# Kernel tuning notes

Hardware: AMD Instinct MI355X
Metric: run time of the kernel (lower is better)

## Reference

```python
import jax, jax.numpy as jnp
import numpy as np

N = 100000
E = 1600000
G = 64  # number of graphs in batch
IN_DIM = 256
HID = 64
HEADS = 4
NUM_DOMAINS = 2
NEG_SLOPE = 0.2


def setup_inputs() -> dict:
    key = jax.random.key(0)
    ks = jax.random.split(key, 16)
    x = jax.random.normal(ks[0], (N, IN_DIM), dtype=jnp.float32)
    edge_index = jax.random.randint(ks[1], (2, E), 0, N, dtype=jnp.int64)
    batch = jnp.sort(jax.random.randint(ks[2], (N,), 0, G, dtype=jnp.int64))
    s = 1.0 / np.sqrt(IN_DIM)
    W1 = jax.random.uniform(ks[3], (IN_DIM, HEADS * HID), jnp.float32, -s, s)
    att_src1 = jax.random.normal(ks[4], (HEADS, HID), jnp.float32) * 0.1
    att_dst1 = jax.random.normal(ks[5], (HEADS, HID), jnp.float32) * 0.1
    b1 = jnp.zeros((HEADS * HID,), jnp.float32)
    s2 = 1.0 / np.sqrt(HEADS * HID)
    W2 = jax.random.uniform(ks[6], (HEADS * HID, HID), jnp.float32, -s2, s2)
    att_src2 = jax.random.normal(ks[7], (1, HID), jnp.float32) * 0.1
    att_dst2 = jax.random.normal(ks[8], (1, HID), jnp.float32) * 0.1
    b2 = jnp.zeros((HID,), jnp.float32)
    s3 = 1.0 / np.sqrt(HID)
    W3 = jax.random.uniform(ks[9], (HID, HID // 2), jnp.float32, -s3, s3)
    b3 = jnp.zeros((HID // 2,), jnp.float32)
    s4 = 1.0 / np.sqrt(HID // 2)
    W4 = jax.random.uniform(ks[10], (HID // 2, NUM_DOMAINS), jnp.float32, -s4, s4)
    b4 = jnp.zeros((NUM_DOMAINS,), jnp.float32)
    return dict(x=x, edge_index=edge_index, batch=batch,
                W1=W1, att_src1=att_src1, att_dst1=att_dst1, b1=b1,
                W2=W2, att_src2=att_src2, att_dst2=att_dst2, b2=b2,
                W3=W3, b3=b3, W4=W4, b4=b4)


def gat_conv(x, src, dst, W, att_src, att_dst, bias, concat):
    # PyG GATConv (dropout inactive in eval mode)
    H, C = att_src.shape
    h = (x @ W).reshape(N, H, C)                      # [N,H,C]
    a_src = jnp.sum(h * att_src, axis=-1)             # [N,H]
    a_dst = jnp.sum(h * att_dst, axis=-1)             # [N,H]
    alpha = jax.nn.leaky_relu(a_src[src] + a_dst[dst], NEG_SLOPE)  # [E',H]
    amax = jax.ops.segment_max(alpha, dst, num_segments=N)
    alpha = jnp.exp(alpha - amax[dst])
    denom = jax.ops.segment_sum(alpha, dst, num_segments=N)
    alpha = alpha / (denom[dst] + 1e-16)              # segment softmax over incoming edges
    msg = h[src] * alpha[..., None]                   # [E',H,C]
    out = jax.ops.segment_sum(msg, dst, num_segments=N)  # [N,H,C]
    if concat:
        return out.reshape(N, H * C) + bias
    return out.mean(axis=1) + bias


def reference(x, edge_index, batch,
              W1, att_src1, att_dst1, b1,
              W2, att_src2, att_dst2, b2,
              W3, b3, W4, b4):
    # GRL is identity in forward
    loops = jnp.arange(N, dtype=edge_index.dtype)
    src = jnp.concatenate([edge_index[0], loops])  # add_self_loops (PyG default)
    dst = jnp.concatenate([edge_index[1], loops])
    h = jax.nn.elu(gat_conv(x, src, dst, W1, att_src1, att_dst1, b1, concat=True))
    h = gat_conv(h, src, dst, W2, att_src2, att_dst2, b2, concat=False)  # [N,HID]
    # global mean pool over graphs
    sums = jax.ops.segment_sum(h, batch, num_segments=G)
    cnt = jax.ops.segment_sum(jnp.ones((N,), h.dtype), batch, num_segments=G)
    graph_emb = sums / jnp.maximum(cnt, 1.0)[:, None]  # [G,HID]
    z = jax.nn.relu(graph_emb @ W3 + b3)
    logits = z @ W4 + b4                                # [G,NUM_DOMAINS]
    return logits
```

## Files before the change

### kernel.cpp

```cpp
#include <hip/hip_runtime.h>
#include <math.h>

#define N_NODES 100000
#define E_EDGES 1600000
#define E_TOT   (E_EDGES + N_NODES)
#define G_GRAPHS 64
#define IN_DIM 256
#define HID 64
#define HEADS 4
#define D1 256
#define NEG_SLOPE 0.2f
#define SCAN_B 1024
#define CHUNK2 8

typedef float nfloat4 __attribute__((ext_vector_type(4)));
typedef unsigned short nus4 __attribute__((ext_vector_type(4)));
typedef short bf16x8 __attribute__((ext_vector_type(8)));
typedef float f32x4 __attribute__((ext_vector_type(4)));

__device__ __forceinline__ float bf2f(unsigned short u) {
    unsigned int t = ((unsigned int)u) << 16;
    return __builtin_bit_cast(float, t);
}
__device__ __forceinline__ unsigned short f2bf(float f) {
    unsigned int u = __builtin_bit_cast(unsigned int, f);
    u += 0x7FFF + ((u >> 16) & 1);
    return (unsigned short)(u >> 16);
}
__device__ __forceinline__ unsigned int pk2(float lo, float hi) {
    unsigned int ul = __builtin_bit_cast(unsigned int, lo) + 0x8000u;
    unsigned int uh = __builtin_bit_cast(unsigned int, hi) + 0x8000u;
    return __builtin_amdgcn_perm(uh, ul, 0x07060302u);
}

__device__ __forceinline__ void packW(const float* __restrict__ W,
                                      unsigned short* __restrict__ Wpk, int Nc, int t)
{
    int kg = t / Nc, n = t - kg * Nc;
    const float* p = W + (size_t)(kg * 8) * Nc + n;
    uint4 v;
    v.x = pk2(p[0],      p[Nc]);
    v.y = pk2(p[2 * Nc], p[3 * Nc]);
    v.z = pk2(p[4 * Nc], p[5 * Nc]);
    v.w = pk2(p[6 * Nc], p[7 * Nc]);
    *(uint4*)(Wpk + (size_t)t * 8) = v;
}
__global__ __launch_bounds__(256) void convW2x(const float* __restrict__ W1,
                                               unsigned short* __restrict__ Wpk1,
                                               const float* __restrict__ W2,
                                               unsigned short* __restrict__ Wpk2)
{
    int t = blockIdx.x * 256 + threadIdx.x;
    if (t < 32 * D1) packW(W1, Wpk1, D1, t);
    else if (t < 32 * D1 + 32 * HID) packW(W2, Wpk2, HID, t - 32 * D1);
}

template<int BN, bool ABF16, bool CFP8>
__global__ __launch_bounds__(256) void gemm_mfma(const void* __restrict__ Ain,
                                                 const unsigned short* __restrict__ Wpk,
                                                 void* __restrict__ C,
                                                 int Nc,
                                                 const float* __restrict__ att_src,
                                                 const float* __restrict__ att_dst,
                                                 float* __restrict__ a_srcO,
                                                 float* __restrict__ a_dstO,
                                                 int astride)
{
    constexpr int NCG = BN / 16;
    __shared__ unsigned short alds[2][4][128][8];
    const int tid = threadIdx.x;
    const int lane = tid & 63, wv = tid >> 6;
    const int qd = lane >> 4, c16 = lane & 15;
    const int bm = blockIdx.y * 128, bn = blockIdx.x * BN;

    f32x4 acc[2][NCG];
#pragma unroll
    for (int i = 0; i < 2; ++i)
#pragma unroll
        for (int j = 0; j < NCG; ++j) acc[i][j] = (f32x4){0.f, 0.f, 0.f, 0.f};

    const int ar = tid >> 1, akh = tid & 1;
    const int gm = bm + ar;
    const bool mv = gm < N_NODES;

    uint4 v0, v1;
    float4 f0, f1, f2, f3;
    if (ABF16) {
        const unsigned short* Ab = (const unsigned short*)Ain + (size_t)gm * 256 + akh * 16;
        v0 = mv ? *(const uint4*)Ab : make_uint4(0, 0, 0, 0);
        v1 = mv ? *(const uint4*)(Ab + 8) : make_uint4(0, 0, 0, 0);
    } else {
        const float* Af = (const float*)Ain + (size_t)gm * 256 + akh * 16;
        if (mv) { f0 = ((const float4*)Af)[0]; f1 = ((const float4*)Af)[1];
                  f2 = ((const float4*)Af)[2]; f3 = ((const float4*)Af)[3]; }
        else { f0 = f1 = f2 = f3 = make_float4(0.f, 0.f, 0.f, 0.f); }
    }

    for (int k0 = 0; k0 < 256; k0 += 32) {
        const int p = (k0 >> 5) & 1;
        if (ABF16) {
            *(uint4*)&alds[p][2 * akh][ar][0] = v0;
            *(uint4*)&alds[p][2 * akh + 1][ar][0] = v1;
        } else {
            uint4 p0 = make_uint4(pk2(f0.x, f0.y), pk2(f0.z, f0.w), pk2(f1.x, f1.y), pk2(f1.z, f1.w));
            uint4 p1 = make_uint4(pk2(f2.x, f2.y), pk2(f2.z, f2.w), pk2(f3.x, f3.y), pk2(f3.z, f3.w));
            *(uint4*)&alds[p][2 * akh][ar][0] = p0;
            *(uint4*)&alds[p][2 * akh + 1][ar][0] = p1;
        }
        __syncthreads();

        if (k0 + 32 < 256) {
            if (ABF16) {
                const unsigned short* Ab = (const unsigned short*)Ain + (size_t)gm * 256 + (k0 + 32) + akh * 16;
                v0 = mv ? *(const uint4*)Ab : make_uint4(0, 0, 0, 0);
                v1 = mv ? *(const uint4*)(Ab + 8) : make_uint4(0, 0, 0, 0);
            } else {
                const float* Af = (const float*)Ain + (size_t)gm * 256 + (k0 + 32) + akh * 16;
                if (mv) { f0 = ((const float4*)Af)[0]; f1 = ((const float4*)Af)[1];
                          f2 = ((const float4*)Af)[2]; f3 = ((const float4*)Af)[3]; }
            }
        }

        const unsigned short* Wq = Wpk + ((size_t)((k0 >> 3) + qd) * Nc + bn) * 8;
        bf16x8 af0 = *(const bf16x8*)&alds[p][qd][wv * 32 + c16][0];
        bf16x8 af1 = *(const bf16x8*)&alds[p][qd][wv * 32 + 16 + c16][0];
#pragma unroll
        for (int cg = 0; cg < NCG; ++cg) {
            bf16x8 bfr = *(const bf16x8*)(Wq + (size_t)(cg * 16 + c16) * 8);
            acc[0][cg] = __builtin_amdgcn_mfma_f32_16x16x32_bf16(af0, bfr, acc[0][cg], 0, 0, 0);
            acc[1][cg] = __builtin_amdgcn_mfma_f32_16x16x32_bf16(af1, bfr, acc[1][cg], 0, 0, 0);
        }
    }

    float sv[NCG], dv[NCG];
#pragma unroll
    for (int cg = 0; cg < NCG; ++cg) {
        sv[cg] = att_src[bn + cg * 16 + c16];
        dv[cg] = att_dst[bn + cg * 16 + c16];
    }
#pragma unroll
    for (int rg = 0; rg < 2; ++rg) {
#pragma unroll
        for (int reg = 0; reg < 4; ++reg) {
            const int m = bm + wv * 32 + rg * 16 + qd * 4 + reg;
#pragma unroll
            for (int hh = 0; hh < NCG / 4; ++hh) {
                float ps = 0.f, pd = 0.f;
#pragma unroll
                for (int cg = 4 * hh; cg < 4 * hh + 4; ++cg) {
                    ps += acc[rg][cg][reg] * sv[cg];
                    pd += acc[rg][cg][reg] * dv[cg];
                }
#pragma unroll
                for (int o = 1; o < 16; o <<= 1) { ps += __shfl_xor(ps, o); pd += __shfl_xor(pd, o); }
                if (c16 == 0 && m < N_NODES) {
                    a_srcO[m * astride + (bn >> 6) + hh] = ps;
                    a_dstO[m * astride + (bn >> 6) + hh] = pd;
                }
            }
            if (m < N_NODES) {
#pragma unroll
                for (int cg = 0; cg < NCG; ++cg) {
                    float val = acc[rg][cg][reg];
                    if (CFP8) {
                        unsigned int q = (unsigned int)__builtin_amdgcn_cvt_pk_fp8_f32(val, val, 0, false);
                        ((unsigned char*)C)[(size_t)m * Nc + bn + cg * 16 + c16] = (unsigned char)q;
                    } else {
                        ((unsigned short*)C)[(size_t)m * Nc + bn + cg * 16 + c16] = f2bf(val);
                    }
                }
            }
        }
    }
}

__global__ void edge_hist(const int* __restrict__ ei, int* __restrict__ deg,
                          int* __restrict__ rank)
{
    for (int e = blockIdx.x * blockDim.x + threadIdx.x; e < E_TOT; e += gridDim.x * blockDim.x) {
        int d = (e < E_EDGES) ? ei[E_EDGES + e] : (e - E_EDGES);
        rank[e] = atomicAdd(&deg[d], 1);
    }
}

__global__ __launch_bounds__(SCAN_B) void scan_block(const int* __restrict__ deg,
                                                     int* __restrict__ incl,
                                                     int* __restrict__ bsum, int n)
{
    __shared__ int s[SCAN_B];
    int i = blockIdx.x * SCAN_B + threadIdx.x;
    int v = (i < n) ? deg[i] : 0;
    s[threadIdx.x] = v;
    __syncthreads();
    for (int off = 1; off < SCAN_B; off <<= 1) {
        int t = (threadIdx.x >= off) ? s[threadIdx.x - off] : 0;
        __syncthreads();
        s[threadIdx.x] += t;
        __syncthreads();
    }
    if (i < n) incl[i] = s[threadIdx.x];
    if (threadIdx.x == SCAN_B - 1) bsum[blockIdx.x] = s[SCAN_B - 1];
}

__global__ void scan_bsum(const int* __restrict__ bsum, int* __restrict__ bex, int nb)
{
    __shared__ int s[128];
    int i = threadIdx.x;
    int v = (i < nb) ? bsum[i] : 0;
    s[i] = v;
    __syncthreads();
    for (int off = 1; off < 128; off <<= 1) {
        int t = (i >= off) ? s[i - off] : 0;
        __syncthreads();
        s[i] += t;
        __syncthreads();
    }
    if (i < nb) bex[i] = s[i] - v;
}

__global__ void finalize_off(const int* __restrict__ deg, const int* __restrict__ incl,
                             const int* __restrict__ bex, int* __restrict__ off, int n)
{
    int i = blockIdx.x * blockDim.x + threadIdx.x;
    if (i < n) off[i] = incl[i] - deg[i] + bex[i / SCAN_B];
}

__global__ void edge_scatter(const int* __restrict__ ei, const int* __restrict__ off,
                             const int* __restrict__ rank, int* __restrict__ csr_src)
{
    for (int e = blockIdx.x * blockDim.x + threadIdx.x; e < E_TOT; e += gridDim.x * blockDim.x) {
        int s = (e < E_EDGES) ? ei[e] : (e - E_EDGES);
        int d = (e < E_EDGES) ? ei[E_EDGES + e] : (e - E_EDGES);
        csr_src[off[d] + rank[e]] = s;
    }
}

__global__ __launch_bounds__(256) void agg1_kernel(const unsigned char* __restrict__ h1b,
                                                   const int* __restrict__ csr_src,
                                                   const int* __restrict__ off,
                                                   const int* __restrict__ deg,
                                                   const float* __restrict__ a_src,
                                                   const float* __restrict__ a_dst,
                                                   const float* __restrict__ b1,
                                                   unsigned short* __restrict__ hEb)
{
    __shared__ int s_sh[4][72];
    __shared__ __align__(16) float ex_sh[4][72][4];
    const int wv = threadIdx.x >> 6, lane = threadIdx.x & 63;
    const int n = blockIdx.x * 4 + wv;
    if (n >= N_NODES) return;
    const int h = lane >> 4;
    const int st = off[n], cnt = deg[n];
    const float4 ad4 = *(const float4*)(a_dst + (size_t)n * 4);

    float4 acc = make_float4(0.f, 0.f, 0.f, 0.f);
    float dsum = 0.f;
    const unsigned char* __restrict__ hb = h1b + lane * 4;

    for (int cb = 0; cb < cnt; cb += 64) {
        const int c0 = st + cb;
        const int m = (cnt - cb < 64) ? (cnt - cb) : 64;

        {
            int s_l = csr_src[c0 + ((lane < m) ? lane : 0)];
            float4 as4 = *(const float4*)(a_src + (size_t)s_l * 4);
            float e0 = as4.x + ad4.x, e1 = as4.y + ad4.y,
                  e2 = as4.z + ad4.z, e3 = as4.w + ad4.w;
            e0 = (e0 > 0.f) ? e0 : NEG_SLOPE * e0;
            e1 = (e1 > 0.f) ? e1 : NEG_SLOPE * e1;
            e2 = (e2 > 0.f) ? e2 : NEG_SLOPE * e2;
            e3 = (e3 > 0.f) ? e3 : NEG_SLOPE * e3;
            float4 exv;
            exv.x = __expf(e0); exv.y = __expf(e1);
            exv.z = __expf(e2); exv.w = __expf(e3);
            if (lane < m) {
                s_sh[wv][lane] = s_l;
                *(float4*)&ex_sh[wv][lane][0] = exv;
            }
            if (lane < 8) {
                s_sh[wv][m + lane] = csr_src[c0];
                *(float4*)&ex_sh[wv][m + lane][0] = make_float4(0.f, 0.f, 0.f, 0.f);
            }
        }

        const int m4 = (m + 3) & ~3;
        int   sR0 = s_sh[wv][0], sR1 = s_sh[wv][1], sR2 = s_sh[wv][2], sR3 = s_sh[wv][3];
        float eR0 = ex_sh[wv][0][h], eR1 = ex_sh[wv][1][h],
              eR2 = ex_sh[wv][2][h], eR3 = ex_sh[wv][3][h];
        unsigned int vR0 = *(const unsigned int*)(hb + (size_t)sR0 * D1);
        unsigned int vR1 = *(const unsigned int*)(hb + (size_t)sR1 * D1);
        unsigned int vR2 = *(const unsigned int*)(hb + (size_t)sR2 * D1);
        unsigned int vR3 = *(const unsigned int*)(hb + (size_t)sR3 * D1);
        for (int j = 0; j < m4; j += 4) {
            int   sN0 = s_sh[wv][j + 4], sN1 = s_sh[wv][j + 5],
                  sN2 = s_sh[wv][j + 6], sN3 = s_sh[wv][j + 7];
            float eN0 = ex_sh[wv][j + 4][h], eN1 = ex_sh[wv][j + 5][h],
                  eN2 = ex_sh[wv][j + 6][h], eN3 = ex_sh[wv][j + 7][h];
            unsigned int vN0 = *(const unsigned int*)(hb + (size_t)sN0 * D1);
            unsigned int vN1 = *(const unsigned int*)(hb + (size_t)sN1 * D1);
            unsigned int vN2 = *(const unsigned int*)(hb + (size_t)sN2 * D1);
            unsigned int vN3 = *(const unsigned int*)(hb + (size_t)sN3 * D1);

            dsum += eR0;
            acc.x += eR0 * __builtin_amdgcn_cvt_f32_fp8((int)vR0, 0);
            acc.y += eR0 * __builtin_amdgcn_cvt_f32_fp8((int)vR0, 1);
            acc.z += eR0 * __builtin_amdgcn_cvt_f32_fp8((int)vR0, 2);
            acc.w += eR0 * __builtin_amdgcn_cvt_f32_fp8((int)vR0, 3);
            dsum += eR1;
            acc.x += eR1 * __builtin_amdgcn_cvt_f32_fp8((int)vR1, 0);
            acc.y += eR1 * __builtin_amdgcn_cvt_f32_fp8((int)vR1, 1);
            acc.z += eR1 * __builtin_amdgcn_cvt_f32_fp8((int)vR1, 2);
            acc.w += eR1 * __builtin_amdgcn_cvt_f32_fp8((int)vR1, 3);
            dsum += eR2;
            acc.x += eR2 * __builtin_amdgcn_cvt_f32_fp8((int)vR2, 0);
            acc.y += eR2 * __builtin_amdgcn_cvt_f32_fp8((int)vR2, 1);
            acc.z += eR2 * __builtin_amdgcn_cvt_f32_fp8((int)vR2, 2);
            acc.w += eR2 * __builtin_amdgcn_cvt_f32_fp8((int)vR2, 3);
            dsum += eR3;
            acc.x += eR3 * __builtin_amdgcn_cvt_f32_fp8((int)vR3, 0);
            acc.y += eR3 * __builtin_amdgcn_cvt_f32_fp8((int)vR3, 1);
            acc.z += eR3 * __builtin_amdgcn_cvt_f32_fp8((int)vR3, 2);
            acc.w += eR3 * __builtin_amdgcn_cvt_f32_fp8((int)vR3, 3);

            sR0 = sN0; sR1 = sN1; sR2 = sN2; sR3 = sN3;
            eR0 = eN0; eR1 = eN1; eR2 = eN2; eR3 = eN3;
            vR0 = vN0; vR1 = vN1; vR2 = vN2; vR3 = vN3;
        }
    }

    const float inv = 1.f / (dsum + 1e-16f);
    float4 bb = *(const float4*)(b1 + lane * 4);
    float ox = acc.x * inv + bb.x;
    float oy = acc.y * inv + bb.y;
    float oz = acc.z * inv + bb.z;
    float ow = acc.w * inv + bb.w;
    ox = (ox > 0.f) ? ox : expm1f(ox);
    oy = (oy > 0.f) ? oy : expm1f(oy);
    oz = (oz > 0.f) ? oz : expm1f(oz);
    ow = (ow > 0.f) ? ow : expm1f(ow);
    nus4 ob = { f2bf(ox), f2bf(oy), f2bf(oz), f2bf(ow) };
    __builtin_nontemporal_store(ob, (nus4*)(hEb + (size_t)n * D1 + lane * 4));
}

__global__ __launch_bounds__(256) void agg2_pool_kernel(const unsigned short* __restrict__ h2b,
                                                        const int* __restrict__ csr_src,
                                                        const int* __restrict__ off,
                                                        const int* __restrict__ deg,
                                                        const float* __restrict__ a_src,
                                                        const float* __restrict__ a_dst,
                                                        const float* __restrict__ b2,
                                                        const int* __restrict__ batch,
                                                        float* __restrict__ pool,
                                                        float* __restrict__ cntg)
{
    __shared__ int   s_sh[4][2][80];
    __shared__ float ex_sh[4][2][80];
    const int wv = threadIdx.x >> 6, lane = threadIdx.x & 63;
    const int q = lane >> 4, ql = lane & 15;
    const int f0 = ql * 4;
    const int wgid = blockIdx.x * 4 + wv;
    const int n0 = wgid * CHUNK2;
    if (n0 >= N_NODES) return;
    const int n1 = (n0 + CHUNK2 < N_NODES) ? n0 + CHUNK2 : N_NODES;
    const float4 bb = *(const float4*)(b2 + f0);
    const unsigned short* __restrict__ hb = h2b + f0;

    float4 pacc = make_float4(0.f, 0.f, 0.f, 0.f);
    float ccur = 0.f;
    int gcur = batch[n0];
    int buf = 0;

    int stP = off[n0], cntP = deg[n0];
    float adP = a_dst[n0];
    {
        const int mP = (cntP < 64) ? cntP : 64;
        int s_l = csr_src[stP + ((lane < mP) ? lane : 0)];
        float a = a_src[s_l] + adP;
        a = (a > 0.f) ? a : NEG_SLOPE * a;
        float ex = __expf(a);
        if (lane < mP) { s_sh[wv][0][lane] = s_l; ex_sh[wv][0][lane] = ex; }
        int sb = __shfl(s_l, 0);
        if (lane < 16) { s_sh[wv][0][mP + lane] = sb; ex_sh[wv][0][mP + lane] = 0.f; }
    }

    for (int n = n0; n < n1; ++n) {
        const int st = stP, cnt = cntP;
        const float adn = adP;

        const bool hasN = (n + 1 < n1);
        int stN = 0, cntN = 0, sN = 0; float aN = 0.f, adN = 0.f;
        if (hasN) {
            stN = off[n + 1]; cntN = deg[n + 1]; adN = a_dst[n + 1];
            const int mN = (cntN < 64) ? cntN : 64;
            sN = csr_src[stN + ((lane < mN) ? lane : 0)];
            aN = a_src[sN];
        }

        float4 acc = make_float4(0.f, 0.f, 0.f, 0.f);
        float dsum = 0.f;

        for (int cb = 0; cb < cnt; cb += 64) {
            const int m = (cnt - cb < 64) ? (cnt - cb) : 64;
            if (cb > 0) {
                int s_l = csr_src[st + cb + ((lane < m) ? lane : 0)];
                float a = a_src[s_l] + adn;
                a = (a > 0.f) ? a : NEG_SLOPE * a;
                float ex = __expf(a);
                if (lane < m) { s_sh[wv][buf][lane] = s_l; ex_sh[wv][buf][lane] = ex; }
                int sb = __shfl(s_l, 0);
                if (lane < 16) { s_sh[wv][buf][m + lane] = sb; ex_sh[wv][buf][m + lane] = 0.f; }
            }

            const int m4 = (m + 3) & ~3;
            int   sA = s_sh[wv][buf][q],      sB = s_sh[wv][buf][q + 4],  sC = s_sh[wv][buf][q + 8];
            float eA = ex_sh[wv][buf][q],     eB = ex_sh[wv][buf][q + 4], eC = ex_sh[wv][buf][q + 8];
            ushort4 vA = *(const ushort4*)(hb + (size_t)sA * HID);
            ushort4 vB = *(const ushort4*)(hb + (size_t)sB * HID);
            ushort4 vC = *(const ushort4*)(hb + (size_t)sC * HID);
            for (int j = 0; j < m4; j += 4) {
                int   sD = s_sh[wv][buf][j + 12 + q];
                float eD = ex_sh[wv][buf][j + 12 + q];
                ushort4 vD = *(const ushort4*)(hb + (size_t)sD * HID);

                dsum += eA;
                acc.x += eA * bf2f(vA.x); acc.y += eA * bf2f(vA.y);
                acc.z += eA * bf2f(vA.z); acc.w += eA * bf2f(vA.w);

                sA = sB; eA = eB; vA = vB;
                sB = sC; eB = eC; vB = vC;
                sC = sD; eC = eD; vC = vD;
            }
        }

        if (hasN) {
            const int mN = (cntN < 64) ? cntN : 64;
            float a = aN + adN;
            a = (a > 0.f) ? a : NEG_SLOPE * a;
            float ex = __expf(a);
            if (lane < mN) { s_sh[wv][buf ^ 1][lane] = sN; ex_sh[wv][buf ^ 1][lane] = ex; }
            int sb = __shfl(sN, 0);
            if (lane < 16) { s_sh[wv][buf ^ 1][mN + lane] = sb; ex_sh[wv][buf ^ 1][mN + lane] = 0.f; }
        }

        dsum  += __shfl_xor(dsum, 16);  dsum  += __shfl_xor(dsum, 32);
        acc.x += __shfl_xor(acc.x, 16); acc.x += __shfl_xor(acc.x, 32);
        acc.y += __shfl_xor(acc.y, 16); acc.y += __shfl_xor(acc.y, 32);
        acc.z += __shfl_xor(acc.z, 16); acc.z += __shfl_xor(acc.z, 32);
        acc.w += __shfl_xor(acc.w, 16); acc.w += __shfl_xor(acc.w, 32);

        const float inv = 1.f / (dsum + 1e-16f);
        float4 v;
        v.x = acc.x * inv + bb.x;
        v.y = acc.y * inv + bb.y;
        v.z = acc.z * inv + bb.z;
        v.w = acc.w * inv + bb.w;

        int g = batch[n];
        if (g != gcur) {
            if (q == 0) {
#if defined(__AMDGCN__)
                unsafeAtomicAdd(&pool[gcur * HID + f0 + 0], pacc.x);
                unsafeAtomicAdd(&pool[gcur * HID + f0 + 1], pacc.y);
                unsafeAtomicAdd(&pool[gcur * HID + f0 + 2], pacc.z);
                unsafeAtomicAdd(&pool[gcur * HID + f0 + 3], pacc.w);
                if (ql == 0) unsafeAtomicAdd(&cntg[gcur], ccur);
#else
                atomicAdd(&pool[gcur * HID + f0 + 0], pacc.x);
                atomicAdd(&pool[gcur * HID + f0 + 1], pacc.y);
                atomicAdd(&pool[gcur * HID + f0 + 2], pacc.z);
                atomicAdd(&pool[gcur * HID + f0 + 3], pacc.w);
                if (ql == 0) atomicAdd(&cntg[gcur], ccur);
#endif
            }
            pacc = make_float4(0.f, 0.f, 0.f, 0.f); ccur = 0.f; gcur = g;
        }
        pacc.x += v.x; pacc.y += v.y; pacc.z += v.z; pacc.w += v.w;
        ccur += 1.f;

        stP = stN; cntP = cntN; adP = adN; buf ^= 1;
    }
    if (q == 0) {
#if defined(__AMDGCN__)
        unsafeAtomicAdd(&pool[gcur * HID + f0 + 0], pacc.x);
        unsafeAtomicAdd(&pool[gcur * HID + f0 + 1], pacc.y);
        unsafeAtomicAdd(&pool[gcur * HID + f0 + 2], pacc.z);
        unsafeAtomicAdd(&pool[gcur * HID + f0 + 3], pacc.w);
        if (ql == 0) unsafeAtomicAdd(&cntg[gcur], ccur);
#else
        atomicAdd(&pool[gcur * HID + f0 + 0], pacc.x);
        atomicAdd(&pool[gcur * HID + f0 + 1], pacc.y);
        atomicAdd(&pool[gcur * HID + f0 + 2], pacc.z);
        atomicAdd(&pool[gcur * HID + f0 + 3], pacc.w);
        if (ql == 0) atomicAdd(&cntg[gcur], ccur);
#endif
    }
}

__global__ __launch_bounds__(64) void head_kernel(const float* __restrict__ pool,
                                                  const float* __restrict__ cntg,
                                                  const float* __restrict__ W3,
                                                  const float* __restrict__ b3,
                                                  const float* __restrict__ W4,
                                                  const float* __restrict__ b4,
                                                  float* __restrict__ out)
{
    const int g = blockIdx.x;
    const int lane = threadIdx.x;
    const float invc = 1.f / fmaxf(cntg[g], 1.f);
    float z = 0.f;
    if (lane < 32) {
        z = b3[lane];
        for (int k = 0; k < HID; ++k)
            z += pool[g * HID + k] * invc * W3[k * 32 + lane];
        z = fmaxf(z, 0.f);
    }
    float p0 = (lane < 32) ? z * W4[lane * 2 + 0] : 0.f;
    float p1 = (lane < 32) ? z * W4[lane * 2 + 1] : 0.f;
#pragma unroll
    for (int o = 1; o < 32; o <<= 1) { p0 += __shfl_xor(p0, o); p1 += __shfl_xor(p1, o); }
    if (lane == 0) { out[g * 2 + 0] = b4[0] + p0; out[g * 2 + 1] = b4[1] + p1; }
}

extern "C" void kernel_launch(void* const* d_in, const int* in_sizes, int n_in,
                              void* d_out, int out_size, void* d_ws, size_t ws_size,
                              hipStream_t stream)
{
    const float* x     = (const float*)d_in[0];
    const int*   ei    = (const int*)d_in[1];
    const int*   batch = (const int*)d_in[2];
    const float* W1    = (const float*)d_in[3];
    const float* as1w  = (const float*)d_in[4];
    const float* ad1w  = (const float*)d_in[5];
    const float* b1    = (const float*)d_in[6];
    const float* W2    = (const float*)d_in[7];
    const float* as2w  = (const float*)d_in[8];
    const float* ad2w  = (const float*)d_in[9];
    const float* b2    = (const float*)d_in[10];
    const float* W3    = (const float*)d_in[11];
    const float* b3    = (const float*)d_in[12];
    const float* W4    = (const float*)d_in[13];
    const float* b4    = (const float*)d_in[14];
    float* out = (float*)d_out;

    char* ws = (char*)d_ws;
    size_t o = 0;
    auto alloc = [&](size_t bytes) -> void* {
        void* p = ws + o;
        o += (bytes + 255) & ~(size_t)255;
        return p;
    };
    unsigned char*  h1b = (unsigned char*)alloc((size_t)N_NODES * D1);
    unsigned short* hEb = (unsigned short*)alloc((size_t)N_NODES * D1 * 2);
    unsigned short* h2b = (unsigned short*)alloc((size_t)N_NODES * HID * 2);
    float* a_s1 = (float*)alloc((size_t)N_NODES * 4 * 4);
    float* a_d1 = (float*)alloc((size_t)N_NODES * 4 * 4);
    float* a_s2 = (float*)alloc((size_t)N_NODES * 4);
    float* a_d2 = (float*)alloc((size_t)N_NODES * 4);
    char*  zbase  = (char*)alloc((size_t)N_NODES * 4 + G_GRAPHS * HID * 4 + G_GRAPHS * 4 + 1024);
    int*   deg    = (int*)zbase;
    float* pool   = (float*)(zbase + (((size_t)N_NODES * 4 + 255) & ~(size_t)255));
    float* cntg   = (float*)((char*)pool + (((size_t)G_GRAPHS * HID * 4 + 255) & ~(size_t)255));
    size_t zspan  = (char*)(cntg + G_GRAPHS) - zbase;
    int*   incl   = (int*)alloc((size_t)N_NODES * 4);
    int*   offv   = (int*)alloc((size_t)N_NODES * 4);
    int*   rank   = (int*)alloc((size_t)E_TOT * 4);
    int*   bsum   = (int*)alloc(128 * 4);
    int*   bex    = (int*)alloc(128 * 4);
    int*   csr    = (int*)alloc((size_t)E_TOT * 4);
    unsigned short* Wpk1 = (unsigned short*)alloc((size_t)32 * D1 * 8 * 2);
    unsigned short* Wpk2 = (unsigned short*)alloc((size_t)32 * HID * 8 * 2);

    (void)hipMemsetAsync(zbase, 0, zspan, stream);

    const int nblk_nodes = (N_NODES + 3) / 4;
    const int nscan = (N_NODES + SCAN_B - 1) / SCAN_B;
    const int nrowblk = (N_NODES + 127) / 128;

    convW2x<<<(32 * D1 + 32 * HID + 255) / 256, 256, 0, stream>>>(W1, Wpk1, W2, Wpk2);

    gemm_mfma<128, false, true><<<dim3(2, nrowblk), 256, 0, stream>>>(
        x, Wpk1, h1b, D1, as1w, ad1w, a_s1, a_d1, 4);

    edge_hist<<<4096, 256, 0, stream>>>(ei, deg, rank);
    scan_block<<<nscan, SCAN_B, 0, stream>>>(deg, incl, bsum, N_NODES);
    scan_bsum<<<1, 128, 0, stream>>>(bsum, bex, nscan);
    finalize_off<<<(N_NODES + 255) / 256, 256, 0, stream>>>(deg, incl, bex, offv, N_NODES);
    edge_scatter<<<4096, 256, 0, stream>>>(ei, offv, rank, csr);

    agg1_kernel<<<nblk_nodes, 256, 0, stream>>>(h1b, csr, offv, deg, a_s1, a_d1, b1, hEb);

    gemm_mfma<64, true, false><<<dim3(1, nrowblk), 256, 0, stream>>>(
        hEb, Wpk2, h2b, HID, as2w, ad2w, a_s2, a_d2, 1);

    const int nwaves2 = (N_NODES + CHUNK2 - 1) / CHUNK2;
    agg2_pool_kernel<<<(nwaves2 + 3) / 4, 256, 0, stream>>>(h2b, csr, offv, deg, a_s2, a_d2, b2, batch, pool, cntg);

    head_kernel<<<G_GRAPHS, 64, 0, stream>>>(pool, cntg, W3, b3, W4, b4, out);
}
```

Before: 584.8 us.

## Software-pipeline layer-2 gather across nodes with two-deep index prefetch

Restructures the agg2_pool kernel so that the first 32 neighbor payload rows of the next node are gathered into registers while the current node is accumulated. CSR indices and attention logits are prefetched two nodes ahead. The shared padding grows to 32 slots so these fixed-size loads stay in bounds. The aim is to hide gather latency across node boundaries, at the cost of more registers and wasted loads for low-degree nodes.

```diff
diff --git a/kernel.cpp b/kernel.cpp
--- a/kernel.cpp
+++ b/kernel.cpp
@@ -353,8 +353,8 @@
                                                         float* __restrict__ pool,
                                                         float* __restrict__ cntg)
 {
-    __shared__ int   s_sh[4][2][80];
-    __shared__ float ex_sh[4][2][80];
+    __shared__ int   s_sh[4][2][96];
+    __shared__ float ex_sh[4][2][96];
     const int wv = threadIdx.x >> 6, lane = threadIdx.x & 63;
     const int q = lane >> 4, ql = lane & 15;
     const int f0 = ql * 4;
@@ -370,76 +370,137 @@
     int gcur = batch[n0];
     int buf = 0;
 
-    int stP = off[n0], cntP = deg[n0];
-    float adP = a_dst[n0];
+    int stC = off[n0], cntC = deg[n0];
+    float adC = a_dst[n0];
     {
-        const int mP = (cntP < 64) ? cntP : 64;
-        int s_l = csr_src[stP + ((lane < mP) ? lane : 0)];
-        float a = a_src[s_l] + adP;
+        const int m = (cntC < 64) ? cntC : 64;
+        int s_l = csr_src[stC + ((lane < m) ? lane : 0)];
+        float a = a_src[s_l] + adC;
         a = (a > 0.f) ? a : NEG_SLOPE * a;
         float ex = __expf(a);
-        if (lane < mP) { s_sh[wv][0][lane] = s_l; ex_sh[wv][0][lane] = ex; }
+        if (lane < m) { s_sh[wv][0][lane] = s_l; ex_sh[wv][0][lane] = ex; }
         int sb = __shfl(s_l, 0);
-        if (lane < 16) { s_sh[wv][0][mP + lane] = sb; ex_sh[wv][0][mP + lane] = 0.f; }
+        if (lane < 32) { s_sh[wv][0][m + lane] = sb; ex_sh[wv][0][m + lane] = 0.f; }
+    }
+    ushort4 pay0, pay1, pay2, pay3, pay4, pay5, pay6, pay7;
+    {
+        int t0 = s_sh[wv][0][q], t1 = s_sh[wv][0][q + 4], t2 = s_sh[wv][0][q + 8], t3 = s_sh[wv][0][q + 12];
+        int t4 = s_sh[wv][0][q + 16], t5 = s_sh[wv][0][q + 20], t6 = s_sh[wv][0][q + 24], t7 = s_sh[wv][0][q + 28];
+        pay0 = *(const ushort4*)(hb + (size_t)t0 * HID);
+        pay1 = *(const ushort4*)(hb + (size_t)t1 * HID);
+        pay2 = *(const ushort4*)(hb + (size_t)t2 * HID);
+        pay3 = *(const ushort4*)(hb + (size_t)t3 * HID);
+        pay4 = *(const ushort4*)(hb + (size_t)t4 * HID);
+        pay5 = *(const ushort4*)(hb + (size_t)t5 * HID);
+        pay6 = *(const ushort4*)(hb + (size_t)t6 * HID);
+        pay7 = *(const ushort4*)(hb + (size_t)t7 * HID);
+    }
+
+    int stN = 0, cntN = 0, sNl = 0; float adN = 0.f, aNl = 0.f;
+    if (n0 + 1 < n1) {
+        stN = off[n0 + 1]; cntN = deg[n0 + 1]; adN = a_dst[n0 + 1];
+        const int mN = (cntN < 64) ? cntN : 64;
+        sNl = csr_src[stN + ((lane < mN) ? lane : 0)];
+        aNl = a_src[sNl];
     }
 
     for (int n = n0; n < n1; ++n) {
-        const int st = stP, cnt = cntP;
-        const float adn = adP;
-
+        const int st = stC, cnt = cntC;
+        const float adn = adC;
         const bool hasN = (n + 1 < n1);
-        int stN = 0, cntN = 0, sN = 0; float aN = 0.f, adN = 0.f;
+        const bool hasN2 = (n + 2 < n1);
+
+        int stN2 = 0, cntN2 = 0, sN2l = 0; float adN2 = 0.f, aN2l = 0.f;
+        if (hasN2) {
+            stN2 = off[n + 2]; cntN2 = deg[n + 2]; adN2 = a_dst[n + 2];
+            const int mN2 = (cntN2 < 64) ? cntN2 : 64;
+            sN2l = csr_src[stN2 + ((lane < mN2) ? lane : 0)];
+            aN2l = a_src[sN2l];
+        }
+
         if (hasN) {
-            stN = off[n + 1]; cntN = deg[n + 1]; adN = a_dst[n + 1];
             const int mN = (cntN < 64) ? cntN : 64;
-            sN = csr_src[stN + ((lane < mN) ? lane : 0)];
-            aN = a_src[sN];
+            float a = aNl + adN;
+            a = (a > 0.f) ? a : NEG_SLOPE * a;
+            float ex = __expf(a);
+            if (lane < mN) { s_sh[wv][buf ^ 1][lane] = sNl; ex_sh[wv][buf ^ 1][lane] = ex; }
+            int sb = __shfl(sNl, 0);
+            if (lane < 32) { s_sh[wv][buf ^ 1][mN + lane] = sb; ex_sh[wv][buf ^ 1][mN + lane] = 0.f; }
+        }
+
+        ushort4 pn0, pn1, pn2, pn3, pn4, pn5, pn6, pn7;
+        if (hasN) {
+            const int* sp = &s_sh[wv][buf ^ 1][0];
+            int t0 = sp[q], t1 = sp[q + 4], t2 = sp[q + 8], t3 = sp[q + 12];
+            int t4 = sp[q + 16], t5 = sp[q + 20], t6 = sp[q + 24], t7 = sp[q + 28];
+            pn0 = *(const ushort4*)(hb + (size_t)t0 * HID);
+            pn1 = *(const ushort4*)(hb + (size_t)t1 * HID);
+            pn2 = *(const ushort4*)(hb + (size_t)t2 * HID);
+            pn3 = *(const ushort4*)(hb + (size_t)t3 * HID);
+            pn4 = *(const ushort4*)(hb + (size_t)t4 * HID);
+            pn5 = *(const ushort4*)(hb + (size_t)t5 * HID);
+            pn6 = *(const ushort4*)(hb + (size_t)t6 * HID);
+            pn7 = *(const ushort4*)(hb + (size_t)t7 * HID);
         }
 
         float4 acc = make_float4(0.f, 0.f, 0.f, 0.f);
         float dsum = 0.f;
-
-        for (int cb = 0; cb < cnt; cb += 64) {
+        {
+            const float* ep = &ex_sh[wv][buf][0];
+            float e0 = ep[q], e1 = ep[q + 4], e2 = ep[q + 8], e3 = ep[q + 12];
+            float e4 = ep[q + 16], e5 = ep[q + 20], e6 = ep[q + 24], e7 = ep[q + 28];
+            dsum += e0;
+            acc.x += e0 * bf2f(pay0.x); acc.y += e0 * bf2f(pay0.y);
+            acc.z += e0 * bf2f(pay0.z); acc.w += e0 * bf2f(pay0.w);
+            dsum += e1;
+            acc.x += e1 * bf2f(pay1.x); acc.y += e1 * bf2f(pay1.y);
+            acc.z += e1 * bf2f(pay1.z); acc.w += e1 * bf2f(pay1.w);
+            dsum += e2;
+            acc.x += e2 * bf2f(pay2.x); acc.y += e2 * bf2f(pay2.y);
+            acc.z += e2 * bf2f(pay2.z); acc.w += e2 * bf2f(pay2.w);
+            dsum += e3;
+            acc.x += e3 * bf2f(pay3.x); acc.y += e3 * bf2f(pay3.y);
+            acc.z += e3 * bf2f(pay3.z); acc.w += e3 * bf2f(pay3.w);
+            dsum += e4;
+            acc.x += e4 * bf2f(pay4.x); acc.y += e4 * bf2f(pay4.y);
+            acc.z += e4 * bf2f(pay4.z); acc.w += e4 * bf2f(pay4.w);
+            dsum += e5;
+            acc.x += e5 * bf2f(pay5.x); acc.y += e5 * bf2f(pay5.y);
+            acc.z += e5 * bf2f(pay5.z); acc.w += e5 * bf2f(pay5.w);
+            dsum += e6;
+            acc.x += e6 * bf2f(pay6.x); acc.y += e6 * bf2f(pay6.y);
+            acc.z += e6 * bf2f(pay6.z); acc.w += e6 * bf2f(pay6.w);
+            dsum += e7;
+            acc.x += e7 * bf2f(pay7.x); acc.y += e7 * bf2f(pay7.y);
+            acc.z += e7 * bf2f(pay7.z); acc.w += e7 * bf2f(pay7.w);
+        }
+        const int mC = (cnt < 64) ? cnt : 64;
+        for (int j = 32; j < mC; j += 4) {
+            int   s = s_sh[wv][buf][j + q];
+            float e = ex_sh[wv][buf][j + q];
+            ushort4 v = *(const ushort4*)(hb + (size_t)s * HID);
+            dsum += e;
+            acc.x += e * bf2f(v.x); acc.y += e * bf2f(v.y);
+            acc.z += e * bf2f(v.z); acc.w += e * bf2f(v.w);
+        }
+        for (int cb = 64; cb < cnt; cb += 64) {
             const int m = (cnt - cb < 64) ? (cnt - cb) : 64;
-            if (cb > 0) {
-                int s_l = csr_src[st + cb + ((lane < m) ? lane : 0)];
-                float a = a_src[s_l] + adn;
-                a = (a > 0.f) ? a : NEG_SLOPE * a;
-                float ex = __expf(a);
-                if (lane < m) { s_sh[wv][buf][lane] = s_l; ex_sh[wv][buf][lane] = ex; }
-                int sb = __shfl(s_l, 0);
-                if (lane < 16) { s_sh[wv][buf][m + lane] = sb; ex_sh[wv][buf][m + lane] = 0.f; }
-            }
-
-            const int m4 = (m + 3) & ~3;
-            int   sA = s_sh[wv][buf][q],      sB = s_sh[wv][buf][q + 4],  sC = s_sh[wv][buf][q + 8];
-            float eA = ex_sh[wv][buf][q],     eB = ex_sh[wv][buf][q + 4], eC = ex_sh[wv][buf][q + 8];
-            ushort4 vA = *(const ushort4*)(hb + (size_t)sA * HID);
-            ushort4 vB = *(const ushort4*)(hb + (size_t)sB * HID);
-            ushort4 vC = *(const ushort4*)(hb + (size_t)sC * HID);
-            for (int j = 0; j < m4; j += 4) {
-                int   sD = s_sh[wv][buf][j + 12 + q];
-                float eD = ex_sh[wv][buf][j + 12 + q];
-                ushort4 vD = *(const ushort4*)(hb + (size_t)sD * HID);
-
-                dsum += eA;
-                acc.x += eA * bf2f(vA.x); acc.y += eA * bf2f(vA.y);
-                acc.z += eA * bf2f(vA.z); acc.w += eA * bf2f(vA.w);
-
-                sA = sB; eA = eB; vA = vB;
-                sB = sC; eB = eC; vB = vC;
-                sC = sD; eC = eD; vC = vD;
-            }
-        }
-
-        if (hasN) {
-            const int mN = (cntN < 64) ? cntN : 64;
-            float a = aN + adN;
+            int s_l = csr_src[st + cb + ((lane < m) ? lane : 0)];
+            float a = a_src[s_l] + adn;
             a = (a > 0.f) ? a : NEG_SLOPE * a;
             float ex = __expf(a);
-            if (lane < mN) { s_sh[wv][buf ^ 1][lane] = sN; ex_sh[wv][buf ^ 1][lane] = ex; }
-            int sb = __shfl(sN, 0);
-            if (lane < 16) { s_sh[wv][buf ^ 1][mN + lane] = sb; ex_sh[wv][buf ^ 1][mN + lane] = 0.f; }
+            if (lane < m) { s_sh[wv][buf][lane] = s_l; ex_sh[wv][buf][lane] = ex; }
+            int sb = __shfl(s_l, 0);
+            if (lane < 32) { s_sh[wv][buf][m + lane] = sb; ex_sh[wv][buf][m + lane] = 0.f; }
+            const int m4 = (m + 3) & ~3;
+            for (int j = 0; j < m4; j += 4) {
+                int   s = s_sh[wv][buf][j + q];
+                float e = ex_sh[wv][buf][j + q];
+                ushort4 v = *(const ushort4*)(hb + (size_t)s * HID);
+                dsum += e;
+                acc.x += e * bf2f(v.x); acc.y += e * bf2f(v.y);
+                acc.z += e * bf2f(v.z); acc.w += e * bf2f(v.w);
+            }
         }
 
         dsum  += __shfl_xor(dsum, 16);  dsum  += __shfl_xor(dsum, 32);
@@ -477,7 +538,14 @@
         pacc.x += v.x; pacc.y += v.y; pacc.z += v.z; pacc.w += v.w;
         ccur += 1.f;
 
-        stP = stN; cntP = cntN; adP = adN; buf ^= 1;
+        stC = stN; cntC = cntN; adC = adN;
+        stN = stN2; cntN = cntN2; adN = adN2;
+        sNl = sN2l; aNl = aN2l;
+        if (hasN) {
+            pay0 = pn0; pay1 = pn1; pay2 = pn2; pay3 = pn3;
+            pay4 = pn4; pay5 = pn5; pay6 = pn6; pay7 = pn7;
+        }
+        buf ^= 1;
     }
     if (q == 0) {
 #if defined(__AMDGCN__)
```

After: 594.8 us. Within noise of the previous version (+1.7%).

## Split layer-2 aggregation and mean pooling into separate per-node and pool kernels

Applied to the files above, without the earlier changes.

The fused aggregation+pooling kernel, where each wave walked 8 nodes with software prefetch, is replaced by a one-wave-per-node aggregation kernel that writes fp32 node outputs to a new buffer. A separate pool kernel then sums those rows per graph with atomics. This aims for more parallelism and better latency hiding in the gather. In exchange it adds an extra kernel launch plus a 25.6MB write and reread, and drops the cross-node prefetch.

```diff
diff --git a/kernel.cpp b/kernel.cpp
--- a/kernel.cpp
+++ b/kernel.cpp
@@ -11,7 +11,6 @@
 #define D1 256
 #define NEG_SLOPE 0.2f
 #define SCAN_B 1024
-#define CHUNK2 8
 
 typedef float nfloat4 __attribute__((ext_vector_type(4)));
 typedef unsigned short nus4 __attribute__((ext_vector_type(4)));
@@ -342,158 +341,117 @@
     __builtin_nontemporal_store(ob, (nus4*)(hEb + (size_t)n * D1 + lane * 4));
 }
 
-__global__ __launch_bounds__(256) void agg2_pool_kernel(const unsigned short* __restrict__ h2b,
+__global__ __launch_bounds__(256) void agg2_node_kernel(const unsigned short* __restrict__ h2b,
                                                         const int* __restrict__ csr_src,
                                                         const int* __restrict__ off,
                                                         const int* __restrict__ deg,
                                                         const float* __restrict__ a_src,
                                                         const float* __restrict__ a_dst,
                                                         const float* __restrict__ b2,
-                                                        const int* __restrict__ batch,
-                                                        float* __restrict__ pool,
-                                                        float* __restrict__ cntg)
-{
-    __shared__ int   s_sh[4][2][80];
-    __shared__ float ex_sh[4][2][80];
+                                                        float* __restrict__ h3)
+{
+    __shared__ int   s_sh[4][96];
+    __shared__ float ex_sh[4][96];
     const int wv = threadIdx.x >> 6, lane = threadIdx.x & 63;
+    const int n = blockIdx.x * 4 + wv;
+    if (n >= N_NODES) return;
     const int q = lane >> 4, ql = lane & 15;
     const int f0 = ql * 4;
-    const int wgid = blockIdx.x * 4 + wv;
-    const int n0 = wgid * CHUNK2;
-    if (n0 >= N_NODES) return;
-    const int n1 = (n0 + CHUNK2 < N_NODES) ? n0 + CHUNK2 : N_NODES;
-    const float4 bb = *(const float4*)(b2 + f0);
+    const int st = off[n], cnt = deg[n];
+    const float adn = a_dst[n];
     const unsigned short* __restrict__ hb = h2b + f0;
 
-    float4 pacc = make_float4(0.f, 0.f, 0.f, 0.f);
-    float ccur = 0.f;
-    int gcur = batch[n0];
-    int buf = 0;
-
-    int stP = off[n0], cntP = deg[n0];
-    float adP = a_dst[n0];
-    {
-        const int mP = (cntP < 64) ? cntP : 64;
-        int s_l = csr_src[stP + ((lane < mP) ? lane : 0)];
-        float a = a_src[s_l] + adP;
-        a = (a > 0.f) ? a : NEG_SLOPE * a;
-        float ex = __expf(a);
-        if (lane < mP) { s_sh[wv][0][lane] = s_l; ex_sh[wv][0][lane] = ex; }
-        int sb = __shfl(s_l, 0);
-        if (lane < 16) { s_sh[wv][0][mP + lane] = sb; ex_sh[wv][0][mP + lane] = 0.f; }
-    }
-
-    for (int n = n0; n < n1; ++n) {
-        const int st = stP, cnt = cntP;
-        const float adn = adP;
-
-        const bool hasN = (n + 1 < n1);
-        int stN = 0, cntN = 0, sN = 0; float aN = 0.f, adN = 0.f;
-        if (hasN) {
-            stN = off[n + 1]; cntN = deg[n + 1]; adN = a_dst[n + 1];
-            const int mN = (cntN < 64) ? cntN : 64;
-            sN = csr_src[stN + ((lane < mN) ? lane : 0)];
-            aN = a_src[sN];
-        }
-
-        float4 acc = make_float4(0.f, 0.f, 0.f, 0.f);
-        float dsum = 0.f;
-
-        for (int cb = 0; cb < cnt; cb += 64) {
-            const int m = (cnt - cb < 64) ? (cnt - cb) : 64;
-            if (cb > 0) {
-                int s_l = csr_src[st + cb + ((lane < m) ? lane : 0)];
-                float a = a_src[s_l] + adn;
-                a = (a > 0.f) ? a : NEG_SLOPE * a;
-                float ex = __expf(a);
-                if (lane < m) { s_sh[wv][buf][lane] = s_l; ex_sh[wv][buf][lane] = ex; }
-                int sb = __shfl(s_l, 0);
-                if (lane < 16) { s_sh[wv][buf][m + lane] = sb; ex_sh[wv][buf][m + lane] = 0.f; }
-            }
-
-            const int m4 = (m + 3) & ~3;
-            int   sA = s_sh[wv][buf][q],      sB = s_sh[wv][buf][q + 4],  sC = s_sh[wv][buf][q + 8];
-            float eA = ex_sh[wv][buf][q],     eB = ex_sh[wv][buf][q + 4], eC = ex_sh[wv][buf][q + 8];
-            ushort4 vA = *(const ushort4*)(hb + (size_t)sA * HID);
-            ushort4 vB = *(const ushort4*)(hb + (size_t)sB * HID);
-            ushort4 vC = *(const ushort4*)(hb + (size_t)sC * HID);
-            for (int j = 0; j < m4; j += 4) {
-                int   sD = s_sh[wv][buf][j + 12 + q];
-                float eD = ex_sh[wv][buf][j + 12 + q];
-                ushort4 vD = *(const ushort4*)(hb + (size_t)sD * HID);
-
-                dsum += eA;
-                acc.x += eA * bf2f(vA.x); acc.y += eA * bf2f(vA.y);
-                acc.z += eA * bf2f(vA.z); acc.w += eA * bf2f(vA.w);
-
-                sA = sB; eA = eB; vA = vB;
-                sB = sC; eB = eC; vB = vC;
-                sC = sD; eC = eD; vC = vD;
-            }
-        }
-
-        if (hasN) {
-            const int mN = (cntN < 64) ? cntN : 64;
-            float a = aN + adN;
+    float4 acc = make_float4(0.f, 0.f, 0.f, 0.f);
+    float dsum = 0.f;
+
+    for (int cb = 0; cb < cnt; cb += 64) {
+        const int c0 = st + cb;
+        const int m = (cnt - cb < 64) ? (cnt - cb) : 64;
+
+        {
+            int s_l = csr_src[c0 + ((lane < m) ? lane : 0)];
+            float a = a_src[s_l] + adn;
             a = (a > 0.f) ? a : NEG_SLOPE * a;
             float ex = __expf(a);
-            if (lane < mN) { s_sh[wv][buf ^ 1][lane] = sN; ex_sh[wv][buf ^ 1][lane] = ex; }
-            int sb = __shfl(sN, 0);
-            if (lane < 16) { s_sh[wv][buf ^ 1][mN + lane] = sb; ex_sh[wv][buf ^ 1][mN + lane] = 0.f; }
-        }
-
-        dsum  += __shfl_xor(dsum, 16);  dsum  += __shfl_xor(dsum, 32);
-        acc.x += __shfl_xor(acc.x, 16); acc.x += __shfl_xor(acc.x, 32);
-        acc.y += __shfl_xor(acc.y, 16); acc.y += __shfl_xor(acc.y, 32);
-        acc.z += __shfl_xor(acc.z, 16); acc.z += __shfl_xor(acc.z, 32);
-        acc.w += __shfl_xor(acc.w, 16); acc.w += __shfl_xor(acc.w, 32);
-
-        const float inv = 1.f / (dsum + 1e-16f);
-        float4 v;
-        v.x = acc.x * inv + bb.x;
-        v.y = acc.y * inv + bb.y;
-        v.z = acc.z * inv + bb.z;
-        v.w = acc.w * inv + bb.w;
-
+            if (lane < m) { s_sh[wv][lane] = s_l; ex_sh[wv][lane] = ex; }
+            int sb = __shfl(s_l, 0);
+            if (lane < 32) { s_sh[wv][m + lane] = sb; ex_sh[wv][m + lane] = 0.f; }
+        }
+
+        const int m4 = (m + 3) & ~3;
+        int   sA = s_sh[wv][q],      sB = s_sh[wv][q + 4],  sC = s_sh[wv][q + 8];
+        float eA = ex_sh[wv][q],     eB = ex_sh[wv][q + 4], eC = ex_sh[wv][q + 8];
+        ushort4 vA = *(const ushort4*)(hb + (size_t)sA * HID);
+        ushort4 vB = *(const ushort4*)(hb + (size_t)sB * HID);
+        ushort4 vC = *(const ushort4*)(hb + (size_t)sC * HID);
+        for (int j = 0; j < m4; j += 4) {
+            int   sD = s_sh[wv][j + 12 + q];
+            float eD = ex_sh[wv][j + 12 + q];
+            ushort4 vD = *(const ushort4*)(hb + (size_t)sD * HID);
+
+            dsum += eA;
+            acc.x += eA * bf2f(vA.x); acc.y += eA * bf2f(vA.y);
+            acc.z += eA * bf2f(vA.z); acc.w += eA * bf2f(vA.w);
+
+            sA = sB; eA = eB; vA = vB;
+            sB = sC; eB = eC; vB = vC;
+            sC = sD; eC = eD; vC = vD;
+        }
+    }
+
+    dsum  += __shfl_xor(dsum, 16);  dsum  += __shfl_xor(dsum, 32);
+    acc.x += __shfl_xor(acc.x, 16); acc.x += __shfl_xor(acc.x, 32);
+    acc.y += __shfl_xor(acc.y, 16); acc.y += __shfl_xor(acc.y, 32);
+    acc.z += __shfl_xor(acc.z, 16); acc.z += __shfl_xor(acc.z, 32);
+    acc.w += __shfl_xor(acc.w, 16); acc.w += __shfl_xor(acc.w, 32);
+
+    const float inv = 1.f / (dsum + 1e-16f);
+    const float4 bb = *(const float4*)(b2 + f0);
+    float4 v;
+    v.x = acc.x * inv + bb.x;
+    v.y = acc.y * inv + bb.y;
+    v.z = acc.z * inv + bb.z;
+    v.w = acc.w * inv + bb.w;
+    if (q == 0)
+        __builtin_nontemporal_store(*(nfloat4*)&v, (nfloat4*)(h3 + (size_t)n * HID + f0));
+}
+
+__global__ __launch_bounds__(256) void pool_kernel(const float* __restrict__ h3,
+                                                   const int* __restrict__ batch,
+                                                   float* __restrict__ pool,
+                                                   float* __restrict__ cntg,
+                                                   int per)
+{
+    const int w = blockIdx.x * 4 + (threadIdx.x >> 6);
+    const int lane = threadIdx.x & 63;
+    const int n0 = w * per;
+    if (n0 >= N_NODES) return;
+    const int n1 = (n0 + per < N_NODES) ? n0 + per : N_NODES;
+
+    float accv = 0.f, c = 0.f;
+    int gcur = batch[n0];
+    for (int n = n0; n < n1; ++n) {
+        float v = h3[(size_t)n * HID + lane];
         int g = batch[n];
         if (g != gcur) {
-            if (q == 0) {
 #if defined(__AMDGCN__)
-                unsafeAtomicAdd(&pool[gcur * HID + f0 + 0], pacc.x);
-                unsafeAtomicAdd(&pool[gcur * HID + f0 + 1], pacc.y);
-                unsafeAtomicAdd(&pool[gcur * HID + f0 + 2], pacc.z);
-                unsafeAtomicAdd(&pool[gcur * HID + f0 + 3], pacc.w);
-                if (ql == 0) unsafeAtomicAdd(&cntg[gcur], ccur);
+            unsafeAtomicAdd(&pool[gcur * HID + lane], accv);
+            if (lane == 0) unsafeAtomicAdd(&cntg[gcur], c);
 #else
-                atomicAdd(&pool[gcur * HID + f0 + 0], pacc.x);
-                atomicAdd(&pool[gcur * HID + f0 + 1], pacc.y);
-                atomicAdd(&pool[gcur * HID + f0 + 2], pacc.z);
-                atomicAdd(&pool[gcur * HID + f0 + 3], pacc.w);
-                if (ql == 0) atomicAdd(&cntg[gcur], ccur);
+            atomicAdd(&pool[gcur * HID + lane], accv);
+            if (lane == 0) atomicAdd(&cntg[gcur], c);
 #endif
-            }
-            pacc = make_float4(0.f, 0.f, 0.f, 0.f); ccur = 0.f; gcur = g;
-        }
-        pacc.x += v.x; pacc.y += v.y; pacc.z += v.z; pacc.w += v.w;
-        ccur += 1.f;
-
-        stP = stN; cntP = cntN; adP = adN; buf ^= 1;
-    }
-    if (q == 0) {
+            accv = 0.f; c = 0.f; gcur = g;
+        }
+        accv += v; c += 1.f;
+    }
 #if defined(__AMDGCN__)
-        unsafeAtomicAdd(&pool[gcur * HID + f0 + 0], pacc.x);
-        unsafeAtomicAdd(&pool[gcur * HID + f0 + 1], pacc.y);
-        unsafeAtomicAdd(&pool[gcur * HID + f0 + 2], pacc.z);
-        unsafeAtomicAdd(&pool[gcur * HID + f0 + 3], pacc.w);
-        if (ql == 0) unsafeAtomicAdd(&cntg[gcur], ccur);
+    unsafeAtomicAdd(&pool[gcur * HID + lane], accv);
+    if (lane == 0) unsafeAtomicAdd(&cntg[gcur], c);
 #else
-        atomicAdd(&pool[gcur * HID + f0 + 0], pacc.x);
-        atomicAdd(&pool[gcur * HID + f0 + 1], pacc.y);
-        atomicAdd(&pool[gcur * HID + f0 + 2], pacc.z);
-        atomicAdd(&pool[gcur * HID + f0 + 3], pacc.w);
-        if (ql == 0) atomicAdd(&cntg[gcur], ccur);
+    atomicAdd(&pool[gcur * HID + lane], accv);
+    if (lane == 0) atomicAdd(&cntg[gcur], c);
 #endif
-    }
 }
 
 __global__ __launch_bounds__(64) void head_kernel(const float* __restrict__ pool,
@@ -552,6 +510,7 @@
     unsigned char*  h1b = (unsigned char*)alloc((size_t)N_NODES * D1);
     unsigned short* hEb = (unsigned short*)alloc((size_t)N_NODES * D1 * 2);
     unsigned short* h2b = (unsigned short*)alloc((size_t)N_NODES * HID * 2);
+    float* h3   = (float*)alloc((size_t)N_NODES * HID * 4);
     float* a_s1 = (float*)alloc((size_t)N_NODES * 4 * 4);
     float* a_d1 = (float*)alloc((size_t)N_NODES * 4 * 4);
     float* a_s2 = (float*)alloc((size_t)N_NODES * 4);
@@ -592,8 +551,11 @@
     gemm_mfma<64, true, false><<<dim3(1, nrowblk), 256, 0, stream>>>(
         hEb, Wpk2, h2b, HID, as2w, ad2w, a_s2, a_d2, 1);
 
-    const int nwaves2 = (N_NODES + CHUNK2 - 1) / CHUNK2;
-    agg2_pool_kernel<<<(nwaves2 + 3) / 4, 256, 0, stream>>>(h2b, csr, offv, deg, a_s2, a_d2, b2, batch, pool, cntg);
+    agg2_node_kernel<<<nblk_nodes, 256, 0, stream>>>(h2b, csr, offv, deg, a_s2, a_d2, b2, h3);
+
+    const int npool_blk = 512;
+    const int per = (N_NODES + npool_blk * 4 - 1) / (npool_blk * 4);
+    pool_kernel<<<npool_blk, 256, 0, stream>>>(h3, batch, pool, cntg, per);
 
     head_kernel<<<G_GRAPHS, 64, 0, stream>>>(pool, cntg, W3, b3, W4, b4, out);
 }
```

Result: faster. 552.0 us (-5.6%).
